# Kernel tuning notes

Hardware: AMD Instinct MI355X
Metric: run time of the kernel (lower is better)

The kernel has to match this reference:

```python
import jax, jax.numpy as jnp
import numpy as np
from jax import lax

B, HW, PS, MP, ED, NH = 32, 256, 16, 20, 64, 4


def _conv(x, w, b):
    y = lax.conv_general_dilated(x, w, (1, 1), 'SAME', dimension_numbers=('NCHW', 'OIHW', 'NCHW'))
    return y + b[None, :, None, None]


def _maxpool2(x):
    return lax.reduce_window(x, -jnp.inf, lax.max, (1, 1, 2, 2), (1, 1, 2, 2), 'VALID')


def _extract(x, c1w, c1b, c2w, c2b, c3w, c3b, c4w, c4b, fcw, fcb):
    # FeatureExtractor: conv-conv-pool, conv-conv-pool, adaptive avg pool (4,4), fc -> 128
    x = x[:, None]  # (B,1,H,W)
    x = jax.nn.relu(_conv(x, c1w, c1b))
    x = jax.nn.relu(_conv(x, c2w, c2b))
    x = _maxpool2(x)
    x = jax.nn.relu(_conv(x, c3w, c3b))
    x = jax.nn.relu(_conv(x, c4w, c4b))
    x = _maxpool2(x)
    b_, c_, h_, w_ = x.shape
    x = x.reshape(b_, c_, 4, h_ // 4, 4, w_ // 4).mean((3, 5))  # AdaptiveAvgPool2d((4,4))
    return x.reshape(b_, -1) @ fcw.T + fcb


def _rope(x):
    # x: (B, heads, S, D); faithful to RotaryPositionalEmbedding (identity at S=1)
    S, D = x.shape[-2], x.shape[-1]
    pos = jnp.arange(S, dtype=jnp.float32)[:, None]
    freqs = jnp.exp(jnp.arange(0, D, 2, dtype=jnp.float32) * (-np.log(10000.0) / D))
    emb = pos * freqs  # (S, D/2)
    cos = jnp.cos(emb)[None, :, None, :]
    sin = jnp.sin(emb)[None, :, None, :]
    x1, x2 = jnp.split(x, 2, axis=-1)
    return jnp.concatenate([x1 * cos - x2 * sin, x1 * sin + x2 * cos], -1)


def _attn(x, wq, wk, wv, wow, wob):
    b_, s_, d_ = x.shape
    hd = d_ // NH
    scale = hd ** -0.5
    def heads(w):
        return (x @ w.T).reshape(b_, s_, NH, hd).transpose(0, 2, 1, 3)
    q, k, v = heads(wq), heads(wk), heads(wv)
    q, k = _rope(q), _rope(k)
    a = jax.nn.softmax(jnp.einsum('bhqd,bhkd->bhqk', q, k) * scale, -1)
    o = jnp.einsum('bhqk,bhkd->bhqd', a, v).transpose(0, 2, 1, 3).reshape(b_, s_, d_)
    return o @ wow.T + wob


def _patch_feats(sig, pew, peb):
    # SignalPatching: row-major stride-8 16x16 patches, first MP=20, embed, mean over patches
    H, W = sig.shape[1], sig.shape[2]
    stride = PS // 2
    pos = [(i, j) for i in range(0, H - PS + 1, stride) for j in range(0, W - PS + 1, stride)][:MP]
    ri = np.array([p[0] for p in pos])[:, None] + np.arange(PS)  # (MP,PS)
    ci = np.array([p[1] for p in pos])[:, None] + np.arange(PS)
    patches = sig[:, ri[:, :, None], ci[:, None, :]]  # (B,MP,PS,PS)
    emb = patches.reshape(sig.shape[0], len(pos), PS * PS) @ pew.T + peb  # (B,MP,ED)
    return emb.mean(1)


def _forward(time_input, freq_input,
             t_c1w, t_c1b, t_c2w, t_c2b, t_c3w, t_c3b, t_c4w, t_c4b, t_fcw, t_fcb,
             t_redw, t_redb, t_wq, t_wk, t_wv, t_wow, t_wob, t_pew, t_peb,
             f_c1w, f_c1b, f_c2w, f_c2b, f_c3w, f_c3b, f_c4w, f_c4b, f_fcw, f_fcb,
             f_redw, f_redb, f_wq, f_wk, f_wv, f_wow, f_wob, f_pew, f_peb,
             c1w, c1b, c2w, c2b, c3w, c3b):
    tf = _extract(time_input, t_c1w, t_c1b, t_c2w, t_c2b, t_c3w, t_c3b, t_c4w, t_c4b, t_fcw, t_fcb)
    tp = _patch_feats(time_input, t_pew, t_peb)
    tr = jax.nn.relu(tf @ t_redw.T + t_redb)  # DimensionalityReducer (eval: dropout off)
    ta = _attn(tr[:, None, :], t_wq, t_wk, t_wv, t_wow, t_wob)[:, 0]
    ff = _extract(freq_input, f_c1w, f_c1b, f_c2w, f_c2b, f_c3w, f_c3b, f_c4w, f_c4b, f_fcw, f_fcb)
    fp = _patch_feats(freq_input, f_pew, f_peb)
    fr = jax.nn.relu(ff @ f_redw.T + f_redb)
    fa = _attn(fr[:, None, :], f_wq, f_wk, f_wv, f_wow, f_wob)[:, 0]
    feats = jnp.concatenate([ta, fa, tp, fp], -1)  # (B, 256)
    h = jax.nn.relu(feats @ c1w.T + c1b)
    h = jax.nn.relu(h @ c2w.T + c2b)
    return h @ c3w.T + c3b  # (B, num_classes)


def setup_inputs() -> dict:
    key = jax.random.key(0)
    ks = iter(jax.random.split(key, 64))
    def nrm(*shape):
        return jax.random.normal(next(ks), shape, jnp.float32) * 0.05
    d = {
        'time_input': jax.random.normal(next(ks), (B, HW, HW), jnp.float32),
        'freq_input': jax.random.normal(next(ks), (B, HW, HW), jnp.float32),
    }
    for p in ('t', 'f'):
        d[p + '_c1w'] = nrm(32, 1, 3, 3); d[p + '_c1b'] = jnp.zeros(32, jnp.float32)
        d[p + '_c2w'] = nrm(32, 32, 3, 3); d[p + '_c2b'] = jnp.zeros(32, jnp.float32)
        d[p + '_c3w'] = nrm(64, 32, 3, 3); d[p + '_c3b'] = jnp.zeros(64, jnp.float32)
        d[p + '_c4w'] = nrm(64, 64, 3, 3); d[p + '_c4b'] = jnp.zeros(64, jnp.float32)
        d[p + '_fcw'] = nrm(128, 64 * 4 * 4); d[p + '_fcb'] = jnp.zeros(128, jnp.float32)
        d[p + '_redw'] = nrm(64, 128); d[p + '_redb'] = jnp.zeros(64, jnp.float32)
        d[p + '_wq'] = nrm(64, 64); d[p + '_wk'] = nrm(64, 64); d[p + '_wv'] = nrm(64, 64)
        d[p + '_wow'] = nrm(64, 64); d[p + '_wob'] = jnp.zeros(64, jnp.float32)
        d[p + '_pew'] = nrm(ED, PS * PS); d[p + '_peb'] = jnp.zeros(ED, jnp.float32)
    d['c1w'] = nrm(256, 256); d['c1b'] = jnp.zeros(256, jnp.float32)
    d['c2w'] = nrm(128, 256); d['c2b'] = jnp.zeros(128, jnp.float32)
    d['c3w'] = nrm(2, 128); d['c3b'] = jnp.zeros(2, jnp.float32)
    return d


def reference(time_input, freq_input,
              t_c1w, t_c1b, t_c2w, t_c2b, t_c3w, t_c3b, t_c4w, t_c4b, t_fcw, t_fcb,
              t_redw, t_redb, t_wq, t_wk, t_wv, t_wow, t_wob, t_pew, t_peb,
              f_c1w, f_c1b, f_c2w, f_c2b, f_c3w, f_c3b, f_c4w, f_c4b, f_fcw, f_fcb,
              f_redw, f_redb, f_wq, f_wk, f_wv, f_wow, f_wob, f_pew, f_peb,
              c1w, c1b, c2w, c2b, c3w, c3b):
    return _forward(time_input, freq_input,
                    t_c1w, t_c1b, t_c2w, t_c2b, t_c3w, t_c3b, t_c4w, t_c4b, t_fcw, t_fcb,
                    t_redw, t_redb, t_wq, t_wk, t_wv, t_wow, t_wob, t_pew, t_peb,
                    f_c1w, f_c1b, f_c2w, f_c2b, f_c3w, f_c3b, f_c4w, f_c4b, f_fcw, f_fcb,
                    f_redw, f_redb, f_wq, f_wk, f_wv, f_wow, f_wob, f_pew, f_peb,
                    c1w, c1b, c2w, c2b, c3w, c3b)
```

## Files before the change

kernel.cpp:

```cpp
#include <hip/hip_runtime.h>


typedef short bf16x8 __attribute__((ext_vector_type(8)));
typedef float f32x4 __attribute__((ext_vector_type(4)));

__device__ __forceinline__ unsigned short bf16_rne(float f) {
    unsigned int u = __float_as_uint(f);
    u += 0x7fffu + ((u >> 16) & 1u);
    return (unsigned short)(u >> 16);
}
__device__ __forceinline__ float bf2f(unsigned short h) {
    unsigned int u = ((unsigned int)h) << 16;
    return __uint_as_float(u);
}

template <int CIN, int COUT>
__global__ void wcvt_kernel(const float* __restrict__ w, unsigned short* __restrict__ wq) {
    int idx = blockIdx.x * 256 + threadIdx.x;
    if (idx >= COUT * CIN * 9) return;
    int ci = idx & 31;
    int co = (idx >> 5) % COUT;
    int r  = (idx >> 5) / COUT;
    int kk = r % 9;
    int cc = r / 9;
    wq[idx] = bf16_rne(w[((size_t)co * CIN + cc * 32 + ci) * 9 + kk]);
}

__global__ void conv1_nhwc_kernel(const float* __restrict__ in, const float* __restrict__ w,
                                  const float* __restrict__ bias, unsigned short* __restrict__ out) {
    __shared__ float xr[3][72];
    __shared__ float ws[288];
    __shared__ float bs[32];
    int x0  = blockIdx.x * 64;
    int y   = blockIdx.y;
    int img = blockIdx.z;
    int tid = threadIdx.x;
    for (int idx = tid; idx < 288; idx += 256) ws[idx] = w[idx];
    if (tid < 32) bs[tid] = bias[tid];
    for (int idx = tid; idx < 3 * 66; idx += 256) {
        int r = idx / 66, c = idx % 66;
        int gy = y - 1 + r, gx = x0 - 1 + c;
        xr[r][c] = (gy >= 0 && gy < 256 && gx >= 0 && gx < 256)
                       ? in[(size_t)img * 65536 + gy * 256 + gx] : 0.f;
    }
    __syncthreads();
    int co = tid & 31, lx = tid >> 5;
    float wk[9];
    #pragma unroll
    for (int k = 0; k < 9; ++k) wk[k] = ws[co * 9 + k];
    float bb = bs[co];
    float xw[3][10];
    #pragma unroll
    for (int r = 0; r < 3; ++r) {
        #pragma unroll
        for (int j = 0; j < 10; ++j) xw[r][j] = xr[r][8 * lx + j];
    }
    unsigned short* op = out + (((size_t)img * 256 + y) * 256 + x0 + 8 * lx) * 32 + co;
    #pragma unroll
    for (int s = 0; s < 8; ++s) {
        float acc = bb;
        #pragma unroll
        for (int ky = 0; ky < 3; ++ky) {
            #pragma unroll
            for (int kx = 0; kx < 3; ++kx) acc = fmaf(wk[ky * 3 + kx], xw[ky][s + kx], acc);
        }
        op[(size_t)s * 32] = bf16_rne(fmaxf(acc, 0.f));
    }
}

template <int CIN, int COUT, int H, bool POOL, int MINW>
__global__ __launch_bounds__(256, MINW) void convmfma_kernel(const unsigned short* __restrict__ in,
                                                             const unsigned short* __restrict__ wq,
                                                             const float* __restrict__ bias,
                                                             unsigned short* __restrict__ out) {
    constexpr int NF = COUT / 16;
    __shared__ __align__(16) unsigned short xls[10][34][40];
    int x0  = blockIdx.x * 32;
    int y0  = blockIdx.y * 8;
    int img = blockIdx.z;
    int tid  = threadIdx.x;
    int lane = tid & 63, wvi = tid >> 6;
    int l15 = lane & 15, q8 = (lane >> 4) << 3;

    f32x4 acc[2][2][NF];
    #pragma unroll
    for (int a = 0; a < 2; ++a)
        #pragma unroll
        for (int b = 0; b < 2; ++b)
            #pragma unroll
            for (int c = 0; c < NF; ++c) acc[a][b][c] = (f32x4){0.f, 0.f, 0.f, 0.f};

    const unsigned short* inI = in + (size_t)img * H * H * CIN;
    bf16x8 bcur[NF], bnxt[NF];

    for (int cc = 0; cc < CIN / 32; ++cc) {
        if (cc) __syncthreads();
        const unsigned short* wqc = wq + (size_t)cc * 9 * COUT * 32;
        #pragma unroll
        for (int nf = 0; nf < NF; ++nf)
            bcur[nf] = *(const bf16x8*)&wqc[((size_t)(nf * 16 + l15)) * 32 + q8];
        for (int idx = tid; idx < 10 * 34 * 4; idx += 256) {
            int row = idx / 136, rem = idx % 136, xx = rem >> 2, c4 = rem & 3;
            int gy = y0 - 1 + row, gx = x0 - 1 + xx;
            uint4 v = {0u, 0u, 0u, 0u};
            if (gy >= 0 && gy < H && gx >= 0 && gx < H)
                v = *(const uint4*)&inI[((size_t)gy * H + gx) * CIN + cc * 32 + c4 * 8];
            *(uint4*)&xls[row][xx][c4 * 8] = v;
        }
        __syncthreads();

        #pragma unroll 1
        for (int kk = 0; kk < 9; ++kk) {
            int ky = kk / 3, kx = kk - ky * 3;
            int kn = (kk < 8) ? kk + 1 : 8;
            #pragma unroll
            for (int nf = 0; nf < NF; ++nf)
                bnxt[nf] = *(const bf16x8*)&wqc[((size_t)kn * COUT + nf * 16 + l15) * 32 + q8];
            #pragma unroll
            for (int yr = 0; yr < 2; ++yr) {
                int row = 2 * wvi + yr + ky;
                #pragma unroll
                for (int mf = 0; mf < 2; ++mf) {
                    bf16x8 a = *(const bf16x8*)&xls[row][mf * 16 + l15 + kx][q8];
                    #pragma unroll
                    for (int nf = 0; nf < NF; ++nf)
                        acc[yr][mf][nf] =
                            __builtin_amdgcn_mfma_f32_16x16x32_bf16(a, bcur[nf], acc[yr][mf][nf], 0, 0, 0);
                }
            }
            #pragma unroll
            for (int nf = 0; nf < NF; ++nf) bcur[nf] = bnxt[nf];
        }
    }

    float bv[NF];
    #pragma unroll
    for (int nf = 0; nf < NF; ++nf) bv[nf] = bias[nf * 16 + l15];

    if constexpr (POOL) {
        constexpr int Wp = H / 2;
        int yp = y0 / 2 + wvi;
        #pragma unroll
        for (int nf = 0; nf < NF; ++nf) {
            int co = nf * 16 + l15;
            #pragma unroll
            for (int mf = 0; mf < 2; ++mf) {
                #pragma unroll
                for (int t = 0; t < 2; ++t) {
                    float m = fmaxf(fmaxf(acc[0][mf][nf][2 * t], acc[0][mf][nf][2 * t + 1]),
                                    fmaxf(acc[1][mf][nf][2 * t], acc[1][mf][nf][2 * t + 1]));
                    m = fmaxf(m + bv[nf], 0.f);
                    int xp = x0 / 2 + mf * 8 + 2 * (lane >> 4) + t;
                    out[(((size_t)img * Wp + yp) * Wp + xp) * COUT + co] = bf16_rne(m);
                }
            }
        }
    } else {
        #pragma unroll
        for (int yr = 0; yr < 2; ++yr) {
            int y = y0 + 2 * wvi + yr;
            #pragma unroll
            for (int mf = 0; mf < 2; ++mf) {
                #pragma unroll
                for (int nf = 0; nf < NF; ++nf) {
                    int co = nf * 16 + l15;
                    #pragma unroll
                    for (int r = 0; r < 4; ++r) {
                        int x = x0 + mf * 16 + 4 * (lane >> 4) + r;
                        out[(((size_t)img * H + y) * H + x) * COUT + co] =
                            bf16_rne(fmaxf(acc[yr][mf][nf][r] + bv[nf], 0.f));
                    }
                }
            }
        }
    }
}

__global__ void avgfc_kernel(const unsigned short* __restrict__ pin, const float* __restrict__ fcw,
                             const float* __restrict__ fcb, float* __restrict__ tf) {
    __shared__ float av[1024];
    int b = blockIdx.x, tid = threadIdx.x;
    const unsigned short* p = pin + (size_t)b * 64 * 64 * 64;
    for (int idx = tid; idx < 1024; idx += 256) {
        int c = idx & 63, pq = idx >> 6, i = pq >> 2, j = pq & 3;
        float s = 0.f;
        for (int r = 0; r < 16; ++r)
            for (int cc2 = 0; cc2 < 16; ++cc2)
                s += bf2f(p[(((size_t)(i * 16 + r) * 64) + (j * 16 + cc2)) * 64 + c]);
        av[c * 16 + pq] = s * (1.f / 256.f);
    }
    __syncthreads();
    if (tid < 128) {
        float s         = fcb[tid];
        const float* wr = fcw + (size_t)tid * 1024;
        for (int i = 0; i < 1024; ++i) s = fmaf(av[i], wr[i], s);
        tf[b * 128 + tid] = s;
    }
}

__global__ void patch_kernel(const float* __restrict__ sig, const float* __restrict__ pew,
                             const float* __restrict__ peb, float* __restrict__ tp) {
    __shared__ float ps[16][168];
    __shared__ float partial[4][64];
    int b   = blockIdx.x;
    int tid = threadIdx.x;
    for (int idx = tid; idx < 16 * 168; idx += 256) {
        int r = idx / 168, c = idx % 168;
        ps[r][c] = sig[(size_t)b * 65536 + r * 256 + c];
    }
    __syncthreads();
    int e = tid & 63, pg = tid >> 6;
    const float* wr = pew + (size_t)e * 256;
    float s = 0.f;
    for (int r = 0; r < 16; ++r) {
        #pragma unroll
        for (int c = 0; c < 16; ++c) {
            float acc = 0.f;
            for (int pi = pg; pi < 20; pi += 4) acc += ps[r][8 * pi + c];
            s = fmaf(acc, wr[r * 16 + c], s);
        }
    }
    partial[pg][e] = s;
    __syncthreads();
    if (tid < 64) {
        tp[b * 64 + tid] =
            (partial[0][tid] + partial[1][tid] + partial[2][tid] + partial[3][tid]) * (1.f / 20.f) +
            peb[tid];
    }
}

__global__ void redattn_kernel(const float* __restrict__ tf, const float* __restrict__ redw,
                               const float* __restrict__ redb, const float* __restrict__ wv,
                               const float* __restrict__ wow, const float* __restrict__ wob,
                               float* __restrict__ ta) {
    __shared__ float stf[128], str_[64], sv[64];
    int b = blockIdx.x, t = threadIdx.x;
    stf[t]      = tf[b * 128 + t];
    stf[t + 64] = tf[b * 128 + 64 + t];
    __syncthreads();
    float s = redb[t];
    for (int i = 0; i < 128; ++i) s = fmaf(stf[i], redw[t * 128 + i], s);
    str_[t] = fmaxf(s, 0.f);
    __syncthreads();
    s = 0.f;
    for (int i = 0; i < 64; ++i) s = fmaf(str_[i], wv[t * 64 + i], s);
    sv[t] = s;
    __syncthreads();
    s = wob[t];
    for (int i = 0; i < 64; ++i) s = fmaf(sv[i], wow[t * 64 + i], s);
    ta[b * 64 + t] = s;
}

__global__ void head_kernel(const float* __restrict__ taT, const float* __restrict__ taF,
                            const float* __restrict__ tpT, const float* __restrict__ tpF,
                            const float* __restrict__ c1w, const float* __restrict__ c1b,
                            const float* __restrict__ c2w, const float* __restrict__ c2b,
                            const float* __restrict__ c3w, const float* __restrict__ c3b,
                            float* __restrict__ outp) {
    __shared__ float f0[256], h1[256], h2[128];
    int b = blockIdx.x, t = threadIdx.x;
    int seg = t >> 6, e = t & 63;
    const float* sp_ = (seg == 0) ? taT : (seg == 1) ? taF : (seg == 2) ? tpT : tpF;
    f0[t] = sp_[b * 64 + e];
    __syncthreads();
    {
        float s = c1b[t];
        for (int i = 0; i < 256; ++i) s = fmaf(f0[i], c1w[t * 256 + i], s);
        h1[t] = fmaxf(s, 0.f);
    }
    __syncthreads();
    if (t < 128) {
        float s = c2b[t];
        for (int i = 0; i < 256; ++i) s = fmaf(h1[i], c2w[t * 256 + i], s);
        h2[t] = fmaxf(s, 0.f);
    }
    __syncthreads();
    if (t < 2) {
        float s = c3b[t];
        for (int i = 0; i < 128; ++i) s = fmaf(h2[i], c3w[t * 128 + i], s);
        outp[b * 2 + t] = s;
    }
}

extern "C" void kernel_launch(void* const* d_in, const int* in_sizes, int n_in,
                              void* d_out, int out_size, void* d_ws, size_t ws_size,
                              hipStream_t stream) {
    constexpr size_t A_PER = 2097152, B_PER = 524288;
    constexpr size_t SMALL_BYTES = 65536 + 262144;

    int CH = 32;
    while (CH > 1 && ((size_t)CH * (A_PER + B_PER) * 2 + SMALL_BYTES) > ws_size) CH >>= 1;
    const int NCHUNK = 32 / CH;

    unsigned short* A  = (unsigned short*)d_ws;
    unsigned short* Bb = A + (size_t)CH * A_PER;
    float* SM = (float*)(Bb + (size_t)CH * B_PER);
    float* tfB[2] = {SM, SM + 4096};
    float* tpB[2] = {SM + 8192, SM + 10240};
    float* taB[2] = {SM + 12288, SM + 14336};
    unsigned short* WQ = (unsigned short*)(SM + 16384);

    for (int br = 0; br < 2; ++br) {
        const float* in   = (const float*)d_in[br];
        const int base    = 2 + br * 19;
        const float* c1w  = (const float*)d_in[base + 0];
        const float* c1b  = (const float*)d_in[base + 1];
        const float* c2w  = (const float*)d_in[base + 2];
        const float* c2b  = (const float*)d_in[base + 3];
        const float* c3w  = (const float*)d_in[base + 4];
        const float* c3b  = (const float*)d_in[base + 5];
        const float* c4w  = (const float*)d_in[base + 6];
        const float* c4b  = (const float*)d_in[base + 7];
        const float* fcw  = (const float*)d_in[base + 8];
        const float* fcb  = (const float*)d_in[base + 9];
        const float* redw = (const float*)d_in[base + 10];
        const float* redb = (const float*)d_in[base + 11];
        const float* wv_  = (const float*)d_in[base + 14];
        const float* wow_ = (const float*)d_in[base + 15];
        const float* wob_ = (const float*)d_in[base + 16];
        const float* pew  = (const float*)d_in[base + 17];
        const float* peb  = (const float*)d_in[base + 18];

        unsigned short* wq2 = WQ + (size_t)br * 64512;
        unsigned short* wq3 = wq2 + 9216;
        unsigned short* wq4 = wq3 + 18432;
        wcvt_kernel<32, 32><<<36, 256, 0, stream>>>(c2w, wq2);
        wcvt_kernel<32, 64><<<72, 256, 0, stream>>>(c3w, wq3);
        wcvt_kernel<64, 64><<<144, 256, 0, stream>>>(c4w, wq4);

        for (int ck = 0; ck < NCHUNK; ++ck) {
            const float* inC = in + (size_t)ck * CH * 65536;
            conv1_nhwc_kernel<<<dim3(4, 256, CH), 256, 0, stream>>>(inC, c1w, c1b, A);
            convmfma_kernel<32, 32, 256, true, 4>
                <<<dim3(8, 32, CH), 256, 0, stream>>>(A, wq2, c2b, Bb);
            convmfma_kernel<32, 64, 128, false, 3>
                <<<dim3(4, 16, CH), 256, 0, stream>>>(Bb, wq3, c3b, A);
            convmfma_kernel<64, 64, 128, true, 3>
                <<<dim3(4, 16, CH), 256, 0, stream>>>(A, wq4, c4b, Bb);
            avgfc_kernel<<<CH, 256, 0, stream>>>(Bb, fcw, fcb, tfB[br] + (size_t)ck * CH * 128);
            patch_kernel<<<CH, 256, 0, stream>>>(inC, pew, peb, tpB[br] + (size_t)ck * CH * 64);
        }
        redattn_kernel<<<32, 64, 0, stream>>>(tfB[br], redw, redb, wv_, wow_, wob_, taB[br]);
    }

    head_kernel<<<32, 256, 0, stream>>>(taB[0], taB[1], tpB[0], tpB[1],
                                        (const float*)d_in[40], (const float*)d_in[41],
                                        (const float*)d_in[42], (const float*)d_in[43],
                                        (const float*)d_in[44], (const float*)d_in[45],
                                        (float*)d_out);
}
```

Measured before the change: 769.4 us.

## Reuse LDS input rows across ky taps and simplify halo tile loading

The 3x3 conv loop is reordered to iterate over kx outermost. Four input rows of A fragments are loaded from LDS once per kx and reused across the three ky taps, which cuts LDS reads from 36 to 24 per channel chunk. The input tile load is split into an unrolled interior pass that needs no x bounds checks, plus a small pass for the left and right halo columns. In exchange, the explicit double-buffered prefetch of weight fragments is dropped, and the extra A registers may raise register pressure.

```diff
diff --git a/kernel.cpp b/kernel.cpp
--- a/kernel.cpp
+++ b/kernel.cpp
@@ -91,17 +91,23 @@
             for (int c = 0; c < NF; ++c) acc[a][b][c] = (f32x4){0.f, 0.f, 0.f, 0.f};
 
     const unsigned short* inI = in + (size_t)img * H * H * CIN;
-    bf16x8 bcur[NF], bnxt[NF];
 
     for (int cc = 0; cc < CIN / 32; ++cc) {
         if (cc) __syncthreads();
-        const unsigned short* wqc = wq + (size_t)cc * 9 * COUT * 32;
-        #pragma unroll
-        for (int nf = 0; nf < NF; ++nf)
-            bcur[nf] = *(const bf16x8*)&wqc[((size_t)(nf * 16 + l15)) * 32 + q8];
-        for (int idx = tid; idx < 10 * 34 * 4; idx += 256) {
-            int row = idx / 136, rem = idx % 136, xx = rem >> 2, c4 = rem & 3;
-            int gy = y0 - 1 + row, gx = x0 - 1 + xx;
+        #pragma unroll
+        for (int it = 0; it < 5; ++it) {
+            int idx = tid + it * 256;
+            int row = idx >> 7, rem = idx & 127, xx = rem >> 2, c4 = rem & 3;
+            int gy = y0 - 1 + row, gx = x0 + xx;
+            uint4 v = {0u, 0u, 0u, 0u};
+            if (gy >= 0 && gy < H)
+                v = *(const uint4*)&inI[((size_t)gy * H + gx) * CIN + cc * 32 + c4 * 8];
+            *(uint4*)&xls[row][xx + 1][c4 * 8] = v;
+        }
+        if (tid < 80) {
+            int row = tid >> 3, side = (tid >> 2) & 1, c4 = tid & 3;
+            int gy = y0 - 1 + row, gx = side ? (x0 + 32) : (x0 - 1);
+            int xx = side ? 33 : 0;
             uint4 v = {0u, 0u, 0u, 0u};
             if (gy >= 0 && gy < H && gx >= 0 && gx < H)
                 v = *(const uint4*)&inI[((size_t)gy * H + gx) * CIN + cc * 32 + c4 * 8];
@@ -109,27 +115,34 @@
         }
         __syncthreads();
 
+        const unsigned short* wqc = wq + (size_t)cc * 9 * COUT * 32;
         #pragma unroll 1
-        for (int kk = 0; kk < 9; ++kk) {
-            int ky = kk / 3, kx = kk - ky * 3;
-            int kn = (kk < 8) ? kk + 1 : 8;
-            #pragma unroll
-            for (int nf = 0; nf < NF; ++nf)
-                bnxt[nf] = *(const bf16x8*)&wqc[((size_t)kn * COUT + nf * 16 + l15) * 32 + q8];
-            #pragma unroll
-            for (int yr = 0; yr < 2; ++yr) {
-                int row = 2 * wvi + yr + ky;
-                #pragma unroll
-                for (int mf = 0; mf < 2; ++mf) {
-                    bf16x8 a = *(const bf16x8*)&xls[row][mf * 16 + l15 + kx][q8];
+        for (int kx = 0; kx < 3; ++kx) {
+            bf16x8 areg[4][2];
+            #pragma unroll
+            for (int r = 0; r < 4; ++r) {
+                #pragma unroll
+                for (int mf = 0; mf < 2; ++mf)
+                    areg[r][mf] = *(const bf16x8*)&xls[2 * wvi + r][mf * 16 + l15 + kx][q8];
+            }
+            #pragma unroll
+            for (int ky = 0; ky < 3; ++ky) {
+                bf16x8 bfr[NF];
+                #pragma unroll
+                for (int nf = 0; nf < NF; ++nf)
+                    bfr[nf] = *(const bf16x8*)
+                        &wqc[((size_t)(ky * 3 + kx) * COUT + nf * 16 + l15) * 32 + q8];
+                #pragma unroll
+                for (int yr = 0; yr < 2; ++yr) {
                     #pragma unroll
-                    for (int nf = 0; nf < NF; ++nf)
-                        acc[yr][mf][nf] =
-                            __builtin_amdgcn_mfma_f32_16x16x32_bf16(a, bcur[nf], acc[yr][mf][nf], 0, 0, 0);
+                    for (int mf = 0; mf < 2; ++mf) {
+                        #pragma unroll
+                        for (int nf = 0; nf < NF; ++nf)
+                            acc[yr][mf][nf] = __builtin_amdgcn_mfma_f32_16x16x32_bf16(
+                                areg[yr + ky][mf], bfr[nf], acc[yr][mf][nf], 0, 0, 0);
+                    }
                 }
             }
-            #pragma unroll
-            for (int nf = 0; nf < NF; ++nf) bcur[nf] = bnxt[nf];
         }
     }
 
```

Result: slower. 789.1 us (+2.6%).
